# Kernel tuning notes

Hardware: AMD Instinct MI355X
Metric: run time of the kernel (lower is better)

## Reference

```python
import jax, jax.numpy as jnp
import numpy as np

EPS = 1e-6

def _resize_mask_nearest(mask, h, w):
    # mask: (B, H, W) float in {0,1} -> (B, 1, h, w), F.interpolate mode='nearest' semantics
    B, H, W = mask.shape
    ih = (jnp.arange(h) * H) // h  # floor(dst * H/h)
    iw = (jnp.arange(w) * W) // w
    m = mask[:, ih][:, :, iw]
    return m[:, None]  # (B,1,h,w)

def masked_avg_pool(feat, mask_rs):
    # feat: (B,C,H,W), mask_rs: (B,1,H,W) -> (B,C)
    num = (feat * mask_rs).sum(axis=(2, 3))
    den = mask_rs.sum(axis=(2, 3)) + EPS
    return num / den

def compute_P(proto_fg, proto_bg, R):
    # proto_*: (B,d); R: (2,d) learnable anchors -> P: (B,d,d)
    B, d = proto_fg.shape
    C = jnp.stack([proto_bg, proto_fg], axis=1)                     # (B,2,d)
    C = C / (jnp.sqrt((C ** 2).sum(axis=2, keepdims=True)) + EPS)
    Rn = R / (jnp.sqrt((R ** 2).sum(axis=1, keepdims=True)) + EPS)  # (2,d)
    Rb = jnp.broadcast_to(Rn[None], (B, 2, d))
    P = jnp.matmul(jnp.linalg.pinv(C), Rb)                          # (B,d,d)
    return jnp.swapaxes(P, 1, 2)

def apply_P_to_feat(P, feat):
    b, d, h, w = feat.shape
    out = jnp.einsum('bij,bjn->bin', P, feat.reshape(b, d, h * w))
    return out.reshape(b, d, h, w)

def masked_topk_tokens(feat, mask_rs, k):
    # feat: (B,C,H,W), mask_rs: (B,1,H,W) -> tokens (B,k,C); deterministic L2-norm top-k
    b, c, h, w = feat.shape
    scores = jnp.sqrt((feat ** 2).sum(axis=1)).reshape(b, -1)       # (B,HW)
    mask_flat = mask_rs.reshape(b, -1)
    valid = mask_flat.sum(axis=1) > 0
    mask_flat = jnp.where(valid[:, None], mask_flat, 1.0)           # fallback_to_full
    scores = jnp.where(mask_flat >= 0.5, scores, -jnp.inf)
    _, idx = jax.lax.top_k(scores, k)                               # (B,k)
    tok = jnp.take_along_axis(feat.reshape(b, c, -1), idx[:, None, :], axis=2)  # (B,C,k)
    return jnp.swapaxes(tok, 1, 2)                                  # (B,k,C)

def setup_inputs() -> dict:
    key = jax.random.key(0)
    ks = jax.random.split(key, 12)
    B, d = 8, 256
    sizes = [(64, 64), (32, 32), (16, 16)]
    inp = {}
    for i, (h, w) in enumerate(sizes):
        inp[f'q{i+1}'] = jax.random.normal(ks[i], (B, d, h, w), jnp.float32)
        inp[f's{i+1}'] = jax.random.normal(ks[3 + i], (B, d, h, w), jnp.float32)
        # kaiming_normal fan_in=d, linear -> std = 1/sqrt(d)
        inp[f'r{i+1}'] = jax.random.normal(ks[6 + i], (2, d), jnp.float32) / jnp.sqrt(jnp.float32(d))
    inp['support_mask'] = jax.random.randint(ks[9], (B, 512, 512), 0, 2, jnp.int32)
    inp['k'] = 32
    return inp

def reference(q1, q2, q3, s1, s2, s3, r1, r2, r3, support_mask, k):
    mask = support_mask.astype(jnp.float32)  # (B,H,W)
    qs = [q1, q2, q3]
    ss = [s1, s2, s3]
    rs = [r1, r2, r3]
    parts_q, parts_s, pfgs, pbgs = [], [], [], []
    mask_rs0 = None
    s_t0 = None
    for li in range(3):
        q, s, R = qs[li], ss[li], rs[li]
        b, d, h, w = s.shape
        mask_rs = _resize_mask_nearest(mask, h, w)
        proto_fg = masked_avg_pool(s, mask_rs)
        proto_bg = masked_avg_pool(s, 1.0 - mask_rs)
        P = compute_P(proto_fg, proto_bg, R)
        q_t = apply_P_to_feat(P, q)
        s_t = apply_P_to_feat(P, s)
        parts_q.append(q_t.reshape(b, d, -1))
        parts_s.append(s_t.reshape(b, d, -1))
        pfgs.append(masked_avg_pool(s_t, mask_rs))
        pbgs.append(masked_avg_pool(s_t, 1.0 - mask_rs))
        if li == 0:
            mask_rs0, s_t0 = mask_rs, s_t
    tokens = masked_topk_tokens(s_t0, mask_rs0, k)  # (B,k,d)
    # pack everything into one (B, d, N) array: q_t flats, s_t flats, fg/bg protos, tokens
    packed = jnp.concatenate(
        parts_q + parts_s
        + [jnp.stack(pfgs, axis=2), jnp.stack(pbgs, axis=2), jnp.swapaxes(tokens, 1, 2)],
        axis=2)
    return packed
```

## Files before the change

### kernel.cpp

```cpp
#include <hip/hip_runtime.h>
#include <math.h>

#define NTOT 10790
#define NTOT2 5395
#define EPSF 1e-6f

__device__ __forceinline__ float block_reduce_sum(float v, float* red) {
    int tid = threadIdx.x;
    red[tid] = v; __syncthreads();
    for (int off = 128; off > 0; off >>= 1) {
        if (tid < off) red[tid] += red[tid + off];
        __syncthreads();
    }
    float r = red[0];
    __syncthreads();
    return r;
}

__device__ __forceinline__ bool kvGreater(float as, int ai, float bs, int bi) {
    return (as > bs) || (as == bs && ai < bi);
}

__device__ __forceinline__ void sort64(float& s, int& i, int lane) {
    #pragma unroll
    for (int k = 2; k <= 64; k <<= 1) {
        #pragma unroll
        for (int j = k >> 1; j > 0; j >>= 1) {
            float os = __shfl_xor(s, j, 64);
            int   oi = __shfl_xor(i, j, 64);
            bool lower = (lane & j) == 0;
            bool blockDesc = (lane & k) == 0;
            bool keepG = (blockDesc == lower);
            bool og = kvGreater(os, oi, s, i);
            if (og == keepG) { s = os; i = oi; }
        }
    }
}

__device__ __forceinline__ void merge64(float& as, int& ai, float bs, int bi, int lane) {
    float rbs = __shfl(bs, 63 - lane, 64);
    int   rbi = __shfl(bi, 63 - lane, 64);
    if (!kvGreater(as, ai, rbs, rbi)) { as = rbs; ai = rbi; }
    #pragma unroll
    for (int j = 32; j > 0; j >>= 1) {
        float os = __shfl_xor(as, j, 64);
        int   oi = __shfl_xor(ai, j, 64);
        bool lower = (lane & j) == 0;
        bool og = kvGreater(os, oi, as, ai);
        if (og == lower) { as = os; ai = oi; }
    }
}

__global__ __launch_bounds__(256) void mask_kernel(const int* __restrict__ mask,
                                                   float* __restrict__ wsm0,
                                                   float* __restrict__ wsm1,
                                                   float* __restrict__ wsm2,
                                                   float* __restrict__ msum) {
    int level = blockIdx.x, b = blockIdx.y, tid = threadIdx.x;
    int h = 64 >> level, w = h, S = 8 << level, HW = h * w;
    float* wsm = (level == 0) ? wsm0 : ((level == 1) ? wsm1 : wsm2);
    const int* mb = mask + (size_t)b * 512 * 512;
    float acc = 0.f;
    for (int n = tid; n < HW; n += 256) {
        int y = n / w, x = n - y * w;
        float mv = (float)mb[y * S * 512 + x * S];
        wsm[b * HW + n] = mv;
        acc += mv;
    }
    __shared__ float red[256];
    float s = block_reduce_sum(acc, red);
    if (tid == 0) msum[b * 3 + level] = s;
}

__global__ __launch_bounds__(256) void sreduce_kernel(const float* __restrict__ s0,
                                                      const float* __restrict__ s1,
                                                      const float* __restrict__ s2,
                                                      const float* __restrict__ wsm0,
                                                      const float* __restrict__ wsm1,
                                                      const float* __restrict__ wsm2,
                                                      float* __restrict__ fgnum,
                                                      float* __restrict__ tot) {
    int c = blockIdx.x, b = blockIdx.y, level = blockIdx.z, tid = threadIdx.x;
    int HW = 4096 >> (2 * level);
    int HW4 = HW >> 2;
    const float* s = (level == 0) ? s0 : ((level == 1) ? s1 : s2);
    const float* wsm = (level == 0) ? wsm0 : ((level == 1) ? wsm1 : wsm2);
    const float4* sb4 = (const float4*)(s + ((size_t)(b * 256) + c) * HW);
    const float4* mb4 = (const float4*)(wsm + (size_t)b * HW);
    float af = 0.f, at = 0.f;
    for (int i = tid; i < HW4; i += 256) {
        float4 x = sb4[i];
        float4 m = mb4[i];
        at += (x.x + x.y) + (x.z + x.w);
        af = fmaf(x.x, m.x, fmaf(x.y, m.y, fmaf(x.z, m.z, fmaf(x.w, m.w, af))));
    }
    __shared__ float redA[256], redB[256];
    redA[tid] = af; redB[tid] = at; __syncthreads();
    for (int off = 128; off > 0; off >>= 1) {
        if (tid < off) { redA[tid] += redA[tid + off]; redB[tid] += redB[tid + off]; }
        __syncthreads();
    }
    if (tid == 0) {
        int base = (level * 8 + b) * 256 + c;
        fgnum[base] = redA[0];
        tot[base]   = redB[0];
    }
}

__global__ __launch_bounds__(256) void protos_kernel(const float* __restrict__ R0p,
                                                     const float* __restrict__ R1p,
                                                     const float* __restrict__ R2p,
                                                     const float* __restrict__ fgnum,
                                                     const float* __restrict__ tot,
                                                     const float* __restrict__ msum,
                                                     float* __restrict__ c0v,
                                                     float* __restrict__ c1v,
                                                     float* __restrict__ rn0v,
                                                     float* __restrict__ rn1v,
                                                     float* __restrict__ minv,
                                                     float* __restrict__ rg) {
    int b = blockIdx.x, level = blockIdx.y, c = threadIdx.x;
    int HW = 4096 >> (2 * level);
    const float* R = (level == 0) ? R0p : ((level == 1) ? R1p : R2p);
    __shared__ float red[256];
    int base = (level * 8 + b) * 256;
    float ms = msum[b * 3 + level];
    float denf = ms + EPSF;
    float denb = ((float)HW - ms) + EPSF;
    float fg = fgnum[base + c];
    float tt = tot[base + c];
    float pf = fg / denf;
    float pb = (tt - fg) / denb;
    float nf = block_reduce_sum(pf * pf, red);
    float nb = block_reduce_sum(pb * pb, red);
    float C1 = pf / (sqrtf(nf) + EPSF);
    float C0 = pb / (sqrtf(nb) + EPSF);
    c0v[base + c] = C0;
    c1v[base + c] = C1;
    float r0 = R[c], r1 = R[256 + c];
    float n0 = block_reduce_sum(r0 * r0, red);
    float n1 = block_reduce_sum(r1 * r1, red);
    float rr = block_reduce_sum(r0 * r1, red);
    float i0 = 1.0f / (sqrtf(n0) + EPSF);
    float i1 = 1.0f / (sqrtf(n1) + EPSF);
    rn0v[base + c] = r0 * i0;
    rn1v[base + c] = r1 * i1;
    float a  = block_reduce_sum(C0 * C0, red);
    float bb = block_reduce_sum(C0 * C1, red);
    float cc = block_reduce_sum(C1 * C1, red);
    if (c == 0) {
        float det = a * cc - bb * bb;
        float id = 1.0f / det;
        float* M = minv + (level * 8 + b) * 4;
        M[0] = cc * id; M[1] = -bb * id; M[2] = -bb * id; M[3] = a * id;
        float* G = rg + (level * 8 + b) * 4;
        G[0] = n0 * i0 * i0;
        G[1] = rr * i0 * i1;
        G[2] = n1 * i1 * i1;
    }
}

__global__ __launch_bounds__(256) void dots_kernel(const float* __restrict__ q0,
                                                   const float* __restrict__ q1,
                                                   const float* __restrict__ q2,
                                                   const float* __restrict__ s0,
                                                   const float* __restrict__ s1,
                                                   const float* __restrict__ s2,
                                                   const float* __restrict__ c0v,
                                                   const float* __restrict__ c1v,
                                                   const float* __restrict__ minv,
                                                   const float* __restrict__ wsm0,
                                                   const float* __restrict__ wsm1,
                                                   const float* __restrict__ wsm2,
                                                   float* __restrict__ ubuf,
                                                   float* __restrict__ partials) {
    int b = blockIdx.y;
    int xb = blockIdx.x;
    int is_s = (xb >= 42);
    if (is_s) xb -= 42;
    int level, blk;
    if (xb < 32)      { level = 0; blk = xb; }
    else if (xb < 40) { level = 1; blk = xb - 32; }
    else              { level = 2; blk = xb - 40; }
    int HW = 4096 >> (2 * level);
    int HW4 = HW >> 2;
    const float* x = is_s ? ((level == 0) ? s0 : ((level == 1) ? s1 : s2))
                          : ((level == 0) ? q0 : ((level == 1) ? q1 : q2));
    const float* wsm = (level == 0) ? wsm0 : ((level == 1) ? wsm1 : wsm2);
    const int qoffs[3] = {0, 4096, 5120};
    const int soffs[3] = {5376, 9472, 10496};
    int col_off = is_s ? soffs[level] : qoffs[level];
    int n0 = blk * 128;
    int tid = threadIdx.x;

    __shared__ float sc0[256], sc1[256];
    __shared__ float st0[8][32][4], st1[8][32][4];
    __shared__ float pred[2][4];
    int base = (level * 8 + b) * 256;
    sc0[tid] = c0v[base + tid];
    sc1[tid] = c1v[base + tid];
    __syncthreads();

    const float4* xb4 = (const float4*)(x + (size_t)(b * 256) * HW);
    int cg = tid >> 5, l = tid & 31;
    size_t idx0 = (size_t)(cg * 32) * HW4 + (n0 >> 2) + l;
    float t0x = 0, t0y = 0, t0z = 0, t0w = 0;
    float t1x = 0, t1y = 0, t1z = 0, t1w = 0;
    #pragma unroll 8
    for (int i = 0; i < 32; i++) {
        int c = cg * 32 + i;
        float4 xv = xb4[idx0 + (size_t)i * HW4];
        float a = sc0[c], bq = sc1[c];
        t0x = fmaf(a, xv.x, t0x); t0y = fmaf(a, xv.y, t0y);
        t0z = fmaf(a, xv.z, t0z); t0w = fmaf(a, xv.w, t0w);
        t1x = fmaf(bq, xv.x, t1x); t1y = fmaf(bq, xv.y, t1y);
        t1z = fmaf(bq, xv.z, t1z); t1w = fmaf(bq, xv.w, t1w);
    }
    st0[cg][l][0] = t0x; st0[cg][l][1] = t0y; st0[cg][l][2] = t0z; st0[cg][l][3] = t0w;
    st1[cg][l][0] = t1x; st1[cg][l][1] = t1y; st1[cg][l][2] = t1z; st1[cg][l][3] = t1w;
    __syncthreads();

    if (tid < 128) {
        int p = tid;
        const float* f0 = &st0[0][p >> 2][p & 3];
        const float* f1 = &st1[0][p >> 2][p & 3];
        float a0 = 0.f, a1 = 0.f;
        #pragma unroll
        for (int g2 = 0; g2 < 8; g2++) {
            a0 += f0[g2 * 128];
            a1 += f1[g2 * 128];
        }
        const float* M = minv + (level * 8 + b) * 4;
        float u0 = M[0] * a0 + M[1] * a1;
        float u1 = M[1] * a0 + M[3] * a1;
        ((float2*)ubuf)[(size_t)b * 10752 + col_off + n0 + p] = make_float2(u0, u1);
        if (is_s) {
            int n = n0 + p;
            float m = wsm[b * HW + n];
            float p0 = m * u0, p1 = m * u1, p2 = u0, p3 = u1;
            for (int off = 32; off > 0; off >>= 1) {
                p0 += __shfl_down(p0, off, 64);
                p1 += __shfl_down(p1, off, 64);
                p2 += __shfl_down(p2, off, 64);
                p3 += __shfl_down(p3, off, 64);
            }
            if ((tid & 63) == 0) {
                int wv = tid >> 6;
                pred[wv][0] = p0; pred[wv][1] = p1;
                pred[wv][2] = p2; pred[wv][3] = p3;
            }
        }
    }
    __syncthreads();
    if (is_s && tid == 0) {
        float* pp = partials + (((level * 8 + b) * 64) + blk) * 4;
        pp[0] = pred[0][0] + pred[1][0];
        pp[1] = pred[0][1] + pred[1][1];
        pp[2] = pred[0][2] + pred[1][2];
        pp[3] = pred[0][3] + pred[1][3];
    }
}

__global__ __launch_bounds__(256) void recon_kernel(float* __restrict__ out,
                                                    const float* __restrict__ rn0v,
                                                    const float* __restrict__ rn1v,
                                                    const float* __restrict__ ubuf) {
    int b = blockIdx.y;
    int xb = blockIdx.x;
    int is_s = (xb >= 42);
    if (is_s) xb -= 42;
    int level, blk;
    if (xb < 32)      { level = 0; blk = xb; }
    else if (xb < 40) { level = 1; blk = xb - 32; }
    else              { level = 2; blk = xb - 40; }
    const int qoffs[3] = {0, 4096, 5120};
    const int soffs[3] = {5376, 9472, 10496};
    int col = (is_s ? soffs[level] : qoffs[level]) + blk * 128;
    int tid = threadIdx.x;
    int base = (level * 8 + b) * 256;

    __shared__ float srn0[256], srn1[256];
    srn0[tid] = rn0v[base + tid];
    srn1[tid] = rn1v[base + tid];
    __syncthreads();

    int slot = tid & 63, g = tid >> 6;
    float4 uq = ((const float4*)ubuf)[(((size_t)b * 10752 + col) >> 1) + slot];
    float2* ob2 = (float2*)out + ((size_t)(b * 256) + g * 64) * NTOT2 + (col >> 1) + slot;
    #pragma unroll 8
    for (int i = 0; i < 64; i++) {
        int c = g * 64 + i;
        float r0 = srn0[c], r1 = srn1[c];
        ob2[(size_t)i * NTOT2] = make_float2(fmaf(r0, uq.x, r1 * uq.y),
                                             fmaf(r0, uq.z, r1 * uq.w));
    }
}

__global__ __launch_bounds__(1024) void final_kernel(float* __restrict__ out,
                                                     const float* __restrict__ ubuf,
                                                     const float* __restrict__ wsm0,
                                                     const float* __restrict__ msum,
                                                     const float* __restrict__ rn0v,
                                                     const float* __restrict__ rn1v,
                                                     const float* __restrict__ rg,
                                                     const float* __restrict__ partials) {
    int b = blockIdx.x, tid = threadIdx.x;
    int w = tid >> 6, lane = tid & 63;
    __shared__ float lds_s[16 * 64];
    __shared__ int   lds_i[16 * 64];
    __shared__ float2 suv[32];
    __shared__ float sA[3][4];

    const float2* ub = (const float2*)ubuf + (size_t)b * 10752 + 5376;
    float A = rg[b * 4 + 0], B = rg[b * 4 + 1], C = rg[b * 4 + 2];
    bool validmask = msum[b * 3 + 0] > 0.0f;

    float as; int ai;
    #pragma unroll
    for (int c4 = 0; c4 < 4; ++c4) {
        int n = (w * 4 + c4) * 64 + lane;
        float2 uv = ub[n];
        float ss = fmaxf(A * uv.x * uv.x + 2.0f * B * uv.x * uv.y + C * uv.y * uv.y, 0.0f);
        float s = sqrtf(ss);
        float m = validmask ? wsm0[b * 4096 + n] : 1.0f;
        s = (m >= 0.5f) ? s : -INFINITY;
        int i = n;
        sort64(s, i, lane);
        if (c4 == 0) { as = s; ai = i; }
        else merge64(as, ai, s, i, lane);
    }
    lds_s[w * 64 + lane] = as;
    lds_i[w * 64 + lane] = ai;
    __syncthreads();

    for (int act = 8; act >= 1; act >>= 1) {
        float ms_; int mi_;
        bool active = (w < act);
        if (active) {
            ms_ = lds_s[(2 * w) * 64 + lane];
            mi_ = lds_i[(2 * w) * 64 + lane];
            float bs_ = lds_s[(2 * w + 1) * 64 + lane];
            int   bi_ = lds_i[(2 * w + 1) * 64 + lane];
            merge64(ms_, mi_, bs_, bi_, lane);
        }
        __syncthreads();
        if (active) {
            lds_s[w * 64 + lane] = ms_;
            lds_i[w * 64 + lane] = mi_;
        }
        __syncthreads();
    }

    if (tid < 32) {
        suv[tid] = ub[lds_i[tid]];
    }
    __syncthreads();

    int c = tid >> 2, qd = tid & 3;
    float r0 = rn0v[b * 256 + c], r1 = rn1v[b * 256 + c];
    float2* o2 = (float2*)out + ((size_t)(b * 256) + c) * NTOT2 + 5379 + qd * 4;
    #pragma unroll
    for (int t = 0; t < 4; ++t) {
        float2 uv0 = suv[qd * 8 + 2 * t];
        float2 uv1 = suv[qd * 8 + 2 * t + 1];
        o2[t] = make_float2(fmaf(r0, uv0.x, r1 * uv0.y),
                            fmaf(r0, uv1.x, r1 * uv1.y));
    }

    if (tid < 3) {
        int lv = tid;
        const int HWl[3] = {4096, 1024, 256};
        const int nbl[3] = {32, 8, 2};
        const float* pp = partials + ((size_t)(lv * 8 + b) * 64) * 4;
        float t0 = 0, t1 = 0, t2 = 0, t3 = 0;
        for (int i = 0; i < nbl[lv]; i++) {
            t0 += pp[i * 4 + 0]; t1 += pp[i * 4 + 1];
            t2 += pp[i * 4 + 2]; t3 += pp[i * 4 + 3];
        }
        float ms = msum[b * 3 + lv];
        float denf = ms + EPSF;
        float denb = ((float)HWl[lv] - ms) + EPSF;
        sA[lv][0] = t0 / denf;
        sA[lv][1] = t1 / denf;
        sA[lv][2] = (t2 - t0) / denb;
        sA[lv][3] = (t3 - t1) / denb;
    }
    __syncthreads();
    if (tid < 768) {
        int lv = tid >> 8, cc = tid & 255;
        int base = (lv * 8 + b) * 256;
        float rr0 = rn0v[base + cc], rr1 = rn1v[base + cc];
        size_t row = ((size_t)(b * 256) + cc) * NTOT;
        out[row + 10752 + lv] = fmaf(rr0, sA[lv][0], rr1 * sA[lv][1]);
        out[row + 10755 + lv] = fmaf(rr0, sA[lv][2], rr1 * sA[lv][3]);
    }
}

extern "C" void kernel_launch(void* const* d_in, const int* in_sizes, int n_in,
                              void* d_out, int out_size, void* d_ws, size_t ws_size,
                              hipStream_t stream) {
    const float* q0 = (const float*)d_in[0];
    const float* s0 = (const float*)d_in[1];
    const float* r0 = (const float*)d_in[2];
    const float* q1 = (const float*)d_in[3];
    const float* s1 = (const float*)d_in[4];
    const float* r1 = (const float*)d_in[5];
    const float* q2 = (const float*)d_in[6];
    const float* s2 = (const float*)d_in[7];
    const float* r2 = (const float*)d_in[8];
    const int* mask = (const int*)d_in[9];
    float* out = (float*)d_out;
    float* W = (float*)d_ws;

    float* wsm0 = W;
    float* wsm1 = W + 32768;
    float* wsm2 = W + 40960;
    float* msum = W + 43008;
    float* fgnum = W + 43040;
    float* tot  = W + 49184;
    float* c0v  = W + 55328;
    float* c1v  = W + 61472;
    float* rn0v = W + 67616;
    float* rn1v = W + 73760;
    float* minv = W + 79904;
    float* rg   = W + 80000;
    float* ubuf = W + 80128;
    float* part = W + 252160;

    mask_kernel<<<dim3(3, 8), 256, 0, stream>>>(mask, wsm0, wsm1, wsm2, msum);

    sreduce_kernel<<<dim3(256, 8, 3), 256, 0, stream>>>(s0, s1, s2, wsm0, wsm1, wsm2,
                                                        fgnum, tot);

    protos_kernel<<<dim3(8, 3), 256, 0, stream>>>(r0, r1, r2, fgnum, tot, msum,
                                                  c0v, c1v, rn0v, rn1v, minv, rg);

    dots_kernel<<<dim3(84, 8), 256, 0, stream>>>(q0, q1, q2, s0, s1, s2,
                                                 c0v, c1v, minv,
                                                 wsm0, wsm1, wsm2, ubuf, part);

    recon_kernel<<<dim3(84, 8), 256, 0, stream>>>(out, rn0v, rn1v, ubuf);

    final_kernel<<<8, 1024, 0, stream>>>(out, ubuf, wsm0, msum, rn0v, rn1v, rg, part);
}
```

Measured before the change: 81.60 us.

## Restructure recon kernel so each wave writes one full output row

The reconstruction kernel now assigns one wavefront per (batch, channel) output row. Each wave streams the whole packed column range of that row, picking the level coefficients per column with selects. Before, each block covered a 128-column tile across 64 channels, so its writes were strided by the row pitch. The aim is longer contiguous store streams and no shared-memory staging or barrier, at the cost of re-reading the ubuf row for every channel (from cache) and some per-column select logic.

New measurement: 83.37 us. 1.02x slower.

```diff
diff --git a/kernel.cpp b/kernel.cpp
--- a/kernel.cpp
+++ b/kernel.cpp
@@ -265,34 +265,27 @@
                                                     const float* __restrict__ rn0v,
                                                     const float* __restrict__ rn1v,
                                                     const float* __restrict__ ubuf) {
-    int b = blockIdx.y;
-    int xb = blockIdx.x;
-    int is_s = (xb >= 42);
-    if (is_s) xb -= 42;
-    int level, blk;
-    if (xb < 32)      { level = 0; blk = xb; }
-    else if (xb < 40) { level = 1; blk = xb - 32; }
-    else              { level = 2; blk = xb - 40; }
-    const int qoffs[3] = {0, 4096, 5120};
-    const int soffs[3] = {5376, 9472, 10496};
-    int col = (is_s ? soffs[level] : qoffs[level]) + blk * 128;
-    int tid = threadIdx.x;
-    int base = (level * 8 + b) * 256;
-
-    __shared__ float srn0[256], srn1[256];
-    srn0[tid] = rn0v[base + tid];
-    srn1[tid] = rn1v[base + tid];
-    __syncthreads();
-
-    int slot = tid & 63, g = tid >> 6;
-    float4 uq = ((const float4*)ubuf)[(((size_t)b * 10752 + col) >> 1) + slot];
-    float2* ob2 = (float2*)out + ((size_t)(b * 256) + g * 64) * NTOT2 + (col >> 1) + slot;
-    #pragma unroll 8
-    for (int i = 0; i < 64; i++) {
-        int c = g * 64 + i;
-        float r0 = srn0[c], r1 = srn1[c];
-        ob2[(size_t)i * NTOT2] = make_float2(fmaf(r0, uq.x, r1 * uq.y),
-                                             fmaf(r0, uq.z, r1 * uq.w));
+    int wid = blockIdx.x * 4 + (threadIdx.x >> 6);
+    int lane = threadIdx.x & 63;
+    int b = wid >> 8, c = wid & 255;
+    float r00 = rn0v[(0 * 8 + b) * 256 + c], r10 = rn1v[(0 * 8 + b) * 256 + c];
+    float r01 = rn0v[(1 * 8 + b) * 256 + c], r11 = rn1v[(1 * 8 + b) * 256 + c];
+    float r02 = rn0v[(2 * 8 + b) * 256 + c], r12 = rn1v[(2 * 8 + b) * 256 + c];
+    const float4* ub4 = (const float4*)ubuf + (size_t)b * 5376;
+    float2* orow = (float2*)out + (size_t)wid * NTOT2;
+    #pragma unroll 6
+    for (int k = 0; k < 42; k++) {
+        int col4 = k * 64 + lane;
+        float4 ua = ub4[2 * col4];
+        float4 ubq = ub4[2 * col4 + 1];
+        int lv = (col4 < 1344) ? ((col4 < 1024) ? 0 : ((col4 < 1280) ? 1 : 2))
+                               : ((col4 < 2368) ? 0 : ((col4 < 2624) ? 1 : 2));
+        float r0 = (lv == 0) ? r00 : ((lv == 1) ? r01 : r02);
+        float r1 = (lv == 0) ? r10 : ((lv == 1) ? r11 : r12);
+        orow[2 * col4]     = make_float2(fmaf(r0, ua.x, r1 * ua.y),
+                                         fmaf(r0, ua.z, r1 * ua.w));
+        orow[2 * col4 + 1] = make_float2(fmaf(r0, ubq.x, r1 * ubq.y),
+                                         fmaf(r0, ubq.z, r1 * ubq.w));
     }
 }
 
@@ -439,7 +432,7 @@
                                                  c0v, c1v, minv,
                                                  wsm0, wsm1, wsm2, ubuf, part);
 
-    recon_kernel<<<dim3(84, 8), 256, 0, stream>>>(out, rn0v, rn1v, ubuf);
+    recon_kernel<<<512, 256, 0, stream>>>(out, rn0v, rn1v, ubuf);
 
     final_kernel<<<8, 1024, 0, stream>>>(out, ubuf, wsm0, msum, rn0v, rn1v, rg, part);
 }
```
